# Kernel optimization log

Hardware: AMD Instinct MI355X
Metric: run time of the kernel (lower is better)

## Reference

```python
import math
import jax, jax.numpy as jnp
import numpy as np

T = 4096          # sequence length
H = 2048          # hidden_size
I = 8192          # intermediate_size = 4*H
LAYER_ID = 1
N_LAYERS = 24
EPS = 1e-5        # layer_norm_epsilon


def setup_inputs() -> dict:
    key = jax.random.key(0)
    ks = jax.random.split(key, 8)
    s = 1.0 / math.sqrt(H)
    si = 1.0 / math.sqrt(I)
    r0 = LAYER_ID / (N_LAYERS - 1)          # ratio_0_to_1
    r1 = 1.0 - LAYER_ID / N_LAYERS          # ratio_1_to_almost_0
    h = jnp.arange(H, dtype=jnp.float32)
    x = h / H
    time_decay = -5.0 + 8.0 * (h / (H - 1)) ** (0.7 + 1.3 * r0)
    zigzag = 0.5 * ((jnp.arange(1, H + 1) % 3).astype(jnp.float32) - 1.0)
    time_first = jnp.full((H,), math.log(0.3), jnp.float32) + zigzag
    tm_key = x ** r1
    tm_value = tm_key + 0.3 * r0
    tm_recep = x ** (0.5 * r1)
    return {
        "hidden": jax.random.normal(ks[0], (T, H), jnp.float32),
        "att_sx": jnp.zeros((H,), jnp.float32),
        "att_aa": jnp.zeros((H,), jnp.float32),
        "att_bb": jnp.zeros((H,), jnp.float32),
        "att_pp": jnp.full((H,), -1e30, jnp.float32),  # log-space -inf init
        "ffd_sx": jnp.zeros((H,), jnp.float32),
        "ln1_scale": jnp.ones((H,), jnp.float32),
        "ln1_bias": jnp.zeros((H,), jnp.float32),
        "ln2_scale": jnp.ones((H,), jnp.float32),
        "ln2_bias": jnp.zeros((H,), jnp.float32),
        "time_decay": time_decay.astype(jnp.float32),
        "time_first": time_first,
        "tm_key": tm_key.astype(jnp.float32),
        "tm_value": tm_value.astype(jnp.float32),
        "tm_recep": tm_recep.astype(jnp.float32),
        "Wk": jax.random.normal(ks[1], (H, H), jnp.float32) * s,
        "Wv": jax.random.normal(ks[2], (H, H), jnp.float32) * s,
        "Wr": jax.random.normal(ks[3], (H, H), jnp.float32) * s,
        "Wo": jax.random.normal(ks[4], (H, H), jnp.float32) * s,
        "ffn_tm_key": (x ** r1).astype(jnp.float32),
        "ffn_tm_recep": (x ** (0.5 * r1)).astype(jnp.float32),
        "Wfk": jax.random.normal(ks[5], (H, I), jnp.float32) * s,
        "Wfr": jax.random.normal(ks[6], (H, H), jnp.float32) * s,
        "Wfv": jax.random.normal(ks[7], (I, H), jnp.float32) * si,
    }


def _ln(x, scale, bias):
    mu = jnp.mean(x, axis=-1, keepdims=True)
    var = jnp.mean(jnp.square(x - mu), axis=-1, keepdims=True)
    return (x - mu) * jax.lax.rsqrt(var + EPS) * scale + bias


def _block(hidden, att_sx, att_aa, att_bb, att_pp, ffd_sx,
           ln1_scale, ln1_bias, ln2_scale, ln2_bias,
           time_decay, time_first, tm_key, tm_value, tm_recep,
           Wk, Wv, Wr, Wo, ffn_tm_key, ffn_tm_recep, Wfk, Wfr, Wfv):
    # ---- attention (WKV) sub-block ----
    x1 = _ln(hidden, ln1_scale, ln1_bias)               # [T,H]
    c_x = jnp.concatenate((att_sx[None, :], x1[:-1, :]), axis=0)  # token shift
    kx = x1 * tm_key + c_x * (1.0 - tm_key)
    vx = x1 * tm_value + c_x * (1.0 - tm_value)
    rx = x1 * tm_recep + c_x * (1.0 - tm_recep)
    r = jax.nn.sigmoid(rx @ Wr)                         # [T,H]
    k = kx @ Wk
    v = vx @ Wv
    w_decay = -jnp.exp(time_decay)                      # [H]

    def step(carry, kv):
        aa, bb, pp = carry
        kk, vv = kv
        ww = time_first + kk
        p = jnp.maximum(pp, ww)
        e1 = jnp.exp(pp - p)
        e2 = jnp.exp(ww - p)
        out_t = (e1 * aa + e2 * vv) / (e1 * bb + e2)
        ww2 = w_decay + pp
        p2 = jnp.maximum(ww2, kk)
        e1b = jnp.exp(ww2 - p2)
        e2b = jnp.exp(kk - p2)
        return (e1b * aa + e2b * vv, e1b * bb + e2b, p2), out_t

    (aa, bb, pp), cx = jax.lax.scan(step, (att_aa, att_bb, att_pp), (k, v))
    attention = x1 + (r * cx) @ Wo                      # inner residual (as in source)
    hidden2 = hidden + attention

    # ---- feed-forward (channel-mix) sub-block ----
    x2 = _ln(hidden2, ln2_scale, ln2_bias)
    sx2 = jnp.concatenate((ffd_sx[None, :], x2[:-1, :]), axis=0)
    fk = x2 * ffn_tm_key + sx2 * (1.0 - ffn_tm_key)
    fr = x2 * ffn_tm_recep + sx2 * (1.0 - ffn_tm_recep)
    rr = jax.nn.sigmoid(fr @ Wfr)
    kk2 = jnp.square(jax.nn.relu(fk @ Wfk))             # [T,I]
    ffn = rr * (kk2 @ Wfv)
    out = hidden2 + ffn
    return out, x1[-1, :], aa, bb, pp, x2[-1, :]


def reference(hidden, att_sx, att_aa, att_bb, att_pp, ffd_sx,
              ln1_scale, ln1_bias, ln2_scale, ln2_bias,
              time_decay, time_first, tm_key, tm_value, tm_recep,
              Wk, Wv, Wr, Wo, ffn_tm_key, ffn_tm_recep, Wfk, Wfr, Wfv):
    return _block(hidden, att_sx, att_aa, att_bb, att_pp, ffd_sx,
                  ln1_scale, ln1_bias, ln2_scale, ln2_bias,
                  time_decay, time_first, tm_key, tm_value, tm_recep,
                  Wk, Wv, Wr, Wo, ffn_tm_key, ffn_tm_recep, Wfk, Wfr, Wfv)
```

## Files before the change

### kernel.cpp

```cpp
#include <hip/hip_runtime.h>

#define T_SEQ 4096
#define HD 2048
#define ID 8192
#define LN_EPS 1e-5f
#define NCH 64
#define CHL 64
#define CHSZ ((size_t)NCH * HD)

typedef __attribute__((ext_vector_type(4))) float f32x4;
typedef __attribute__((ext_vector_type(8))) short short8;
typedef __attribute__((ext_vector_type(4))) unsigned short ushort4v;

#define GLB(p) ((const __attribute__((address_space(1))) void*)(p))
#define LDSP(p) ((__attribute__((address_space(3))) void*)(p))

__device__ __forceinline__ unsigned short f2bf(float f) {
  union { float f; unsigned int u; } x; x.f = f;
  unsigned int r = x.u + 0x7fffu + ((x.u >> 16) & 1u);
  return (unsigned short)(r >> 16);
}
__device__ __forceinline__ float bf2f(unsigned short u) {
  union { unsigned int i; float f; } x; x.i = ((unsigned int)u) << 16;
  return x.f;
}

__device__ __forceinline__ void wt_body(const float* __restrict__ W,
                                        unsigned short* __restrict__ Wt,
                                        int Nfull, int k_base, int n_base, int Kout) {
  __shared__ float tile[64][65];
  int tx = threadIdx.x, ty = threadIdx.y;
  int n0 = blockIdx.x * 64, k0 = blockIdx.y * 64;
#pragma unroll
  for (int j = 0; j < 8; ++j) {
    int k = ty + 8 * j;
    tile[k][tx] = W[(size_t)(k_base + k0 + k) * Nfull + n_base + n0 + tx];
  }
  __syncthreads();
#pragma unroll
  for (int j = 0; j < 8; ++j) {
    int n = ty + 8 * j;
    Wt[(size_t)(n0 + n) * Kout + k0 + tx] = f2bf(tile[tx][n]);
  }
}

__global__ void k_wt(const float* __restrict__ W, unsigned short* __restrict__ Wt) {
  wt_body(W, Wt, HD, 0, 0, HD);
}

__global__ void k_wt4(const float* __restrict__ W0, const float* __restrict__ W1,
                      const float* __restrict__ W2, const float* __restrict__ W3,
                      unsigned short* __restrict__ T) {
  const float* W = W0;
  if (blockIdx.z == 1) W = W1;
  else if (blockIdx.z == 2) W = W2;
  else if (blockIdx.z == 3) W = W3;
  wt_body(W, T + (size_t)blockIdx.z * HD * HD, HD, 0, 0, HD);
}

__global__ void k_wtB(const float* __restrict__ W, unsigned short* __restrict__ Wt,
                      int Nfull, int Kout, int kbz, int nbz, long dstz) {
  int z = blockIdx.z;
  wt_body(W, Wt + (size_t)z * dstz, Nfull, z * kbz, z * nbz, Kout);
}

__global__ void k_ln(const float* __restrict__ x, const float* __restrict__ sc,
                     const float* __restrict__ bi, unsigned short* __restrict__ y,
                     float* __restrict__ lastrow) {
  int row = blockIdx.x, tid = threadIdx.x;
  const float* xr = x + (size_t)row * HD;
  f32x4 v0 = *(const f32x4*)(xr + tid * 4);
  f32x4 v1 = *(const f32x4*)(xr + 1024 + tid * 4);
  float s = 0.f, s2 = 0.f;
#pragma unroll
  for (int q = 0; q < 4; ++q) { s += v0[q] + v1[q]; s2 += v0[q] * v0[q] + v1[q] * v1[q]; }
#pragma unroll
  for (int o = 32; o; o >>= 1) { s += __shfl_xor(s, o); s2 += __shfl_xor(s2, o); }
  __shared__ float red[8];
  int wv = tid >> 6;
  if ((tid & 63) == 0) { red[wv] = s; red[4 + wv] = s2; }
  __syncthreads();
  if (tid == 0) {
    float a = red[0] + red[1] + red[2] + red[3];
    float b = red[4] + red[5] + red[6] + red[7];
    float mu = a * (1.f / HD);
    float var = b * (1.f / HD) - mu * mu;
    red[0] = mu; red[1] = rsqrtf(var + LN_EPS);
  }
  __syncthreads();
  float mu = red[0], rs = red[1];
  f32x4 s0 = *(const f32x4*)(sc + tid * 4), s1 = *(const f32x4*)(sc + 1024 + tid * 4);
  f32x4 b0 = *(const f32x4*)(bi + tid * 4), b1 = *(const f32x4*)(bi + 1024 + tid * 4);
  float o0[4], o1[4];
  ushort4v y0, y1;
#pragma unroll
  for (int q = 0; q < 4; ++q) {
    o0[q] = (v0[q] - mu) * rs * s0[q] + b0[q];
    o1[q] = (v1[q] - mu) * rs * s1[q] + b1[q];
    y0[q] = f2bf(o0[q]); y1[q] = f2bf(o1[q]);
  }
  unsigned short* yr = y + (size_t)row * HD;
  *(ushort4v*)(yr + tid * 4) = y0;
  *(ushort4v*)(yr + 1024 + tid * 4) = y1;
  if (row == T_SEQ - 1) {
#pragma unroll
    for (int q = 0; q < 4; ++q) {
      lastrow[tid * 4 + q] = o0[q];
      lastrow[1024 + tid * 4 + q] = o1[q];
    }
  }
}

__global__ void k_mix_att(const unsigned short* __restrict__ x1, const float* __restrict__ sx,
                          const float* __restrict__ tk, const float* __restrict__ tv,
                          const float* __restrict__ tr,
                          unsigned short* __restrict__ kx, unsigned short* __restrict__ vx,
                          unsigned short* __restrict__ rx) {
  size_t idx = ((size_t)blockIdx.x * 256 + threadIdx.x) * 4;
  int h = (int)(idx & (HD - 1));
  ushort4v xu = *(const ushort4v*)(x1 + idx);
  f32x4 x, c;
#pragma unroll
  for (int q = 0; q < 4; ++q) x[q] = bf2f(xu[q]);
  if (idx >= HD) {
    ushort4v cu = *(const ushort4v*)(x1 + idx - HD);
#pragma unroll
    for (int q = 0; q < 4; ++q) c[q] = bf2f(cu[q]);
  } else {
    c = *(const f32x4*)(sx + h);
  }
  f32x4 a = *(const f32x4*)(tk + h);
  f32x4 b = *(const f32x4*)(tv + h);
  f32x4 r = *(const f32x4*)(tr + h);
  ushort4v ok, ov, orr;
#pragma unroll
  for (int q = 0; q < 4; ++q) {
    ok[q] = f2bf(x[q] * a[q] + c[q] * (1.f - a[q]));
    ov[q] = f2bf(x[q] * b[q] + c[q] * (1.f - b[q]));
    orr[q] = f2bf(x[q] * r[q] + c[q] * (1.f - r[q]));
  }
  *(ushort4v*)(kx + idx) = ok;
  *(ushort4v*)(vx + idx) = ov;
  *(ushort4v*)(rx + idx) = orr;
}

__global__ void k_mix_ffn(const unsigned short* __restrict__ x2, const float* __restrict__ sx,
                          const float* __restrict__ tk, const float* __restrict__ tr,
                          unsigned short* __restrict__ fk, unsigned short* __restrict__ fr) {
  size_t idx = ((size_t)blockIdx.x * 256 + threadIdx.x) * 4;
  int h = (int)(idx & (HD - 1));
  ushort4v xu = *(const ushort4v*)(x2 + idx);
  f32x4 x, c;
#pragma unroll
  for (int q = 0; q < 4; ++q) x[q] = bf2f(xu[q]);
  if (idx >= HD) {
    ushort4v cu = *(const ushort4v*)(x2 + idx - HD);
#pragma unroll
    for (int q = 0; q < 4; ++q) c[q] = bf2f(cu[q]);
  } else {
    c = *(const f32x4*)(sx + h);
  }
  f32x4 a = *(const f32x4*)(tk + h);
  f32x4 r = *(const f32x4*)(tr + h);
  ushort4v ok, orr;
#pragma unroll
  for (int q = 0; q < 4; ++q) {
    ok[q] = f2bf(x[q] * a[q] + c[q] * (1.f - a[q]));
    orr[q] = f2bf(x[q] * r[q] + c[q] * (1.f - r[q]));
  }
  *(ushort4v*)(fk + idx) = ok;
  *(ushort4v*)(fr + idx) = orr;
}

__global__ void k_scan1(const unsigned short* __restrict__ kb,
                        const unsigned short* __restrict__ vb,
                        const float* __restrict__ td, float* __restrict__ scr) {
  int c = blockIdx.x >> 3;
  int h = (blockIdx.x & 7) * 256 + threadIdx.x;
  float wd = -__expf(td[h]);
  float a = 0.f, b = 0.f, p = -1e30f;
  size_t base = (size_t)c * CHL * HD + h;
#pragma unroll 4
  for (int u = 0; u < CHL; ++u) {
    float kk = bf2f(kb[base]), vv = bf2f(vb[base]);
    base += HD;
    float ww2 = wd + p;
    float p2 = fmaxf(ww2, kk);
    float e1 = __expf(ww2 - p2), e2 = __expf(kk - p2);
    a = e1 * a + e2 * vv;
    b = e1 * b + e2;
    p = p2;
  }
  size_t i = (size_t)c * HD + h;
  scr[i] = a;
  scr[CHSZ + i] = b;
  scr[2 * CHSZ + i] = p;
}

__global__ void k_scan2(const float* __restrict__ scr, float* __restrict__ stscr,
                        const float* __restrict__ aa0, const float* __restrict__ bb0,
                        const float* __restrict__ pp0, const float* __restrict__ td,
                        float* __restrict__ st) {
  int h = blockIdx.x * 256 + threadIdx.x;
  float aa = aa0[h], bb = bb0[h], pp = pp0[h];
  float wdL = -__expf(td[h]) * (float)CHL;
  for (int c = 0; c < NCH; ++c) {
    size_t i = (size_t)c * HD + h;
    stscr[i] = aa;
    stscr[CHSZ + i] = bb;
    stscr[2 * CHSZ + i] = pp;
    float ca = scr[i], cb = scr[CHSZ + i], cp = scr[2 * CHSZ + i];
    float ww2 = wdL + pp;
    float p2 = fmaxf(ww2, cp);
    float e1 = __expf(ww2 - p2), e2 = __expf(cp - p2);
    aa = e1 * aa + e2 * ca;
    bb = e1 * bb + e2 * cb;
    pp = p2;
  }
  st[HD + h] = aa;
  st[2 * HD + h] = bb;
  st[3 * HD + h] = pp;
}

__global__ void k_scan3(const unsigned short* __restrict__ kb,
                        const unsigned short* __restrict__ vb,
                        const unsigned short* __restrict__ rb,
                        const float* __restrict__ tf_, const float* __restrict__ td,
                        const float* __restrict__ stscr, unsigned short* __restrict__ rcx) {
  int c = blockIdx.x >> 3;
  int h = (blockIdx.x & 7) * 256 + threadIdx.x;
  size_t i0 = (size_t)c * HD + h;
  float aa = stscr[i0], bb = stscr[CHSZ + i0], pp = stscr[2 * CHSZ + i0];
  float tf = tf_[h];
  float wd = -__expf(td[h]);
  size_t base = (size_t)c * CHL * HD + h;
#pragma unroll 4
  for (int u = 0; u < CHL; ++u) {
    float kk = bf2f(kb[base]), vv = bf2f(vb[base]), rv = bf2f(rb[base]);
    float ww = tf + kk;
    float p = fmaxf(pp, ww);
    float e1 = __expf(pp - p), e2 = __expf(ww - p);
    float cx = (e1 * aa + e2 * vv) / (e1 * bb + e2);
    rcx[base] = f2bf(rv * cx);
    float ww2 = wd + pp;
    float p2 = fmaxf(ww2, kk);
    float e1b = __expf(ww2 - p2), e2b = __expf(kk - p2);
    aa = e1b * aa + e2b * vv;
    bb = e1b * bb + e2b;
    pp = p2;
    base += HD;
  }
}

__global__ void k_fvred(float* __restrict__ out, const unsigned short* __restrict__ p0,
                        const unsigned short* __restrict__ p1) {
  size_t i = ((size_t)blockIdx.x * 256 + threadIdx.x) * 4;
  f32x4 o = *(f32x4*)(out + i);
  ushort4v a = *(const ushort4v*)(p0 + i);
  ushort4v b = *(const ushort4v*)(p1 + i);
#pragma unroll
  for (int q = 0; q < 4; ++q) o[q] += bf2f(a[q]) + bf2f(b[q]);
  *(f32x4*)(out + i) = o;
}

#define MFMA_Q(mh, nh, bset)                                                   \
  _Pragma("unroll") for (int i_ = 0; i_ < 4; ++i_)                             \
  _Pragma("unroll") for (int j_ = 0; j_ < 2; ++j_)                             \
  _Pragma("unroll") for (int ks_ = 0; ks_ < 2; ++ks_)                          \
    acc[(mh)*4 + i_][(nh)*2 + j_] = __builtin_amdgcn_mfma_f32_16x16x32_bf16(   \
        aS[i_ * 2 + ks_], bset[j_ * 2 + ks_], acc[(mh)*4 + i_][(nh)*2 + j_], 0, 0, 0);

#define RD_A(mh)                                                               \
  { const char* pa_ = Ab + arow0 + (mh)*8192;                                  \
    aS[0] = *(const short8*)(pa_ + 0 * 2048 + swz0);                           \
    aS[1] = *(const short8*)(pa_ + 0 * 2048 + swz1);                           \
    aS[2] = *(const short8*)(pa_ + 1 * 2048 + swz0);                           \
    aS[3] = *(const short8*)(pa_ + 1 * 2048 + swz1);                           \
    aS[4] = *(const short8*)(pa_ + 2 * 2048 + swz0);                           \
    aS[5] = *(const short8*)(pa_ + 2 * 2048 + swz1);                           \
    aS[6] = *(const short8*)(pa_ + 3 * 2048 + swz0);                           \
    aS[7] = *(const short8*)(pa_ + 3 * 2048 + swz1); }

#define RD_B(arr, nh)                                                          \
  { const char* pb_ = Bb + brow0 + (nh)*4096;                                  \
    arr[0] = *(const short8*)(pb_ + 0 * 2048 + swz0);                          \
    arr[1] = *(const short8*)(pb_ + 0 * 2048 + swz1);                          \
    arr[2] = *(const short8*)(pb_ + 1 * 2048 + swz0);                          \
    arr[3] = *(const short8*)(pb_ + 1 * 2048 + swz1); }

template <int EPI>
__global__ __launch_bounds__(512, 2) void k_gemm256(
    const unsigned short* __restrict__ A, const unsigned short* __restrict__ A1,
    const unsigned short* __restrict__ A2,
    const unsigned short* __restrict__ Bt, const unsigned short* __restrict__ Bt1,
    const unsigned short* __restrict__ Bt2,
    int M, int N, int K, int lda, int ldb,
    unsigned short* __restrict__ Cb, unsigned short* __restrict__ Cb1,
    unsigned short* __restrict__ Cb2, const unsigned short* __restrict__ E0b) {
  int koff = 0;
  if (EPI == 10) {
    koff = blockIdx.z * K;
    if (blockIdx.z) Cb = Cb1;
  } else {
    if (blockIdx.z == 1) { A = A1; Bt = Bt1; Cb = Cb1; }
    else if (blockIdx.z == 2) { A = A2; Bt = Bt2; Cb = Cb2; }
  }
  __shared__ char lds[131072];
  int tid = threadIdx.x;
  int wid = tid >> 6, lane = tid & 63;
  int row_l = lane & 15, kg = lane >> 4;
  int warp_m = wid >> 2, warp_n = wid & 3;
  int m0 = blockIdx.x * 256, n0 = blockIdx.y * 256;

  f32x4 acc[8][4];
#pragma unroll
  for (int i = 0; i < 8; ++i)
#pragma unroll
    for (int j = 0; j < 4; ++j)
#pragma unroll
      for (int q = 0; q < 4; ++q) acc[i][j][q] = 0.f;

  int srow = tid >> 3;
  int schunk = (tid & 7) ^ (srow & 7);
  const unsigned short* Asrc = A + (size_t)(m0 + srow) * lda + koff + schunk * 8;
  const unsigned short* Bsrc = Bt + (size_t)(n0 + srow) * ldb + koff + schunk * 8;
  char* ldsw = lds + wid * 1024;

  auto STAGE_A = [&](int d, int kt) {
#pragma unroll
    for (int h = 0; h < 2; ++h) {
      const unsigned short* s = Asrc + (size_t)(h * 128) * lda + kt;
      char* dst = ldsw + d * 65536 + h * 16384;
      __builtin_amdgcn_global_load_lds(GLB(s), LDSP(dst), 16, 0, 0);
      __builtin_amdgcn_global_load_lds(GLB(s + (size_t)64 * lda), LDSP(dst + 8192), 16, 0, 0);
    }
  };
  auto STAGE_B = [&](int d, int kt) {
#pragma unroll
    for (int h = 0; h < 2; ++h) {
      const unsigned short* s = Bsrc + (size_t)(h * 128) * ldb + kt;
      char* dst = ldsw + d * 65536 + 32768 + h * 16384;
      __builtin_amdgcn_global_load_lds(GLB(s), LDSP(dst), 16, 0, 0);
      __builtin_amdgcn_global_load_lds(GLB(s + (size_t)64 * ldb), LDSP(dst + 8192), 16, 0, 0);
    }
  };

  int swz0 = ((kg) ^ (row_l & 7)) << 4;
  int swz1 = ((4 + kg) ^ (row_l & 7)) << 4;
  int arow0 = (warp_m * 128 + row_l) * 128;
  int brow0 = (warp_n * 64 + row_l) * 128;

  short8 aS[8], b0[4], b1[4];
  int nt = K >> 6;
  STAGE_A(0, 0);
  STAGE_B(0, 0);

#pragma unroll 1
  for (int t = 0; t < nt; ++t) {
    int d = t & 1;
    const char* Ab = lds + d * 65536;
    const char* Bb = lds + d * 65536 + 32768;
    bool pre = (t + 1 < nt);
    int kn = (t + 1) << 6;
    if (pre) {
      STAGE_A(d ^ 1, kn);
      asm volatile("s_waitcnt vmcnt(4)" ::: "memory");
    } else {
      asm volatile("s_waitcnt vmcnt(0)" ::: "memory");
    }
    __builtin_amdgcn_s_barrier();
    RD_A(0)
    RD_B(b0, 0)
    asm volatile("s_waitcnt lgkmcnt(0)" ::: "memory");
    __builtin_amdgcn_s_setprio(1);
    MFMA_Q(0, 0, b0)
    __builtin_amdgcn_s_setprio(0);
    __builtin_amdgcn_s_barrier();
    if (pre) STAGE_B(d ^ 1, kn);
    RD_B(b1, 1)
    asm volatile("s_waitcnt lgkmcnt(0)" ::: "memory");
    __builtin_amdgcn_s_setprio(1);
    MFMA_Q(0, 1, b1)
    __builtin_amdgcn_s_setprio(0);
    __builtin_amdgcn_s_barrier();
    RD_A(1)
    asm volatile("s_waitcnt lgkmcnt(0)" ::: "memory");
    __builtin_amdgcn_s_setprio(1);
    MFMA_Q(1, 1, b1)
    __builtin_amdgcn_s_setprio(0);
    __builtin_amdgcn_s_barrier();
    __builtin_amdgcn_s_setprio(1);
    MFMA_Q(1, 0, b0)
    __builtin_amdgcn_s_setprio(0);
    __builtin_amdgcn_s_barrier();
  }

#pragma unroll
  for (int i = 0; i < 8; ++i) {
#pragma unroll
    for (int j = 0; j < 4; ++j) {
#pragma unroll
      for (int q = 0; q < 4; ++q) {
        int r = m0 + warp_m * 128 + i * 16 + kg * 4 + q;
        int c = n0 + warp_n * 64 + j * 16 + row_l;
        size_t idx = (size_t)r * N + c;
        float val = acc[i][j][q];
        if (EPI == 2) { float t2 = val > 0.f ? val * val : 0.f; Cb[idx] = f2bf(t2); }
        if (EPI == 8) {
          float o = (blockIdx.z == 2) ? 1.f / (1.f + __expf(-val)) : val;
          Cb[idx] = f2bf(o);
        }
        if (EPI == 10) Cb[idx] = f2bf(bf2f(E0b[idx]) * val);
      }
    }
  }
}

template <int EPI>
__global__ __launch_bounds__(512) void k_gemmB(
    const unsigned short* __restrict__ A, const unsigned short* __restrict__ Bt,
    int M, int N, int K, int lda, float* __restrict__ C,
    unsigned short* __restrict__ Cb, const float* __restrict__ E0,
    const unsigned short* __restrict__ E1b, const unsigned short* __restrict__ E0b) {
  __shared__ char lds[147456];
  int tid = threadIdx.x;
  int wid = tid >> 6, lane = tid & 63;
  int row_l = lane & 15, kg = lane >> 4;
  int warp_m = wid >> 2, warp_n = wid & 3;
  int m0 = blockIdx.x * 128, n0 = blockIdx.y * 256;

  f32x4 acc[4][4];
#pragma unroll
  for (int i = 0; i < 4; ++i)
#pragma unroll
    for (int j = 0; j < 4; ++j)
#pragma unroll
      for (int q = 0; q < 4; ++q) acc[i][j][q] = 0.f;

  int srow = tid >> 3;
  int schunk = (tid & 7) ^ (srow & 7);
  const unsigned short* Asrc = A + (size_t)(m0 + srow) * lda + schunk * 8;
  const unsigned short* Bsrc = Bt + (size_t)(n0 + srow) * K + schunk * 8;
  int wsw = wid * 1024;

  auto STAGE_P1 = [&](int d, int kt) {
    char* base = lds + d * 49152;
    __builtin_amdgcn_global_load_lds(GLB(Asrc + kt), LDSP(base + wsw), 16, 0, 0);
    __builtin_amdgcn_global_load_lds(GLB(Asrc + (size_t)64 * lda + kt),
                                     LDSP(base + 8192 + wsw), 16, 0, 0);
    __builtin_amdgcn_global_load_lds(GLB(Bsrc + kt), LDSP(base + 16384 + wsw), 16, 0, 0);
  };
  auto STAGE_P2 = [&](int d, int kt) {
    char* base = lds + d * 49152;
#pragma unroll
    for (int h = 1; h < 4; ++h)
      __builtin_amdgcn_global_load_lds(GLB(Bsrc + (size_t)(h * 64) * K + kt),
                                       LDSP(base + 16384 + h * 8192 + wsw), 16, 0, 0);
  };

  int swz0 = ((kg) ^ (row_l & 7)) << 4;
  int swz1 = ((4 + kg) ^ (row_l & 7)) << 4;
  int arow0 = (warp_m * 64 + row_l) * 128;
  int brow0 = (warp_n * 64 + row_l) * 128;

  short8 aS[8], b0[4], b1[4];
  int nt = K >> 6;
  STAGE_P1(0, 0); STAGE_P2(0, 0);
  STAGE_P1(1, 64); STAGE_P2(1, 64);

#pragma unroll 1
  for (int t = 0; t < nt; ++t) {
    int d = t % 3;
    const char* Ab = lds + d * 49152;
    const char* Bb = lds + d * 49152 + 16384;
    int b2 = t + 2 < nt ? (t + 2) % 3 : 0;
    int k2 = (t + 2) << 6;
    if (t + 2 < nt) {
      STAGE_P1(b2, k2);
      asm volatile("s_waitcnt vmcnt(9)" ::: "memory");
    } else if (t + 1 < nt) {
      asm volatile("s_waitcnt vmcnt(6)" ::: "memory");
    } else {
      asm volatile("s_waitcnt vmcnt(0)" ::: "memory");
    }
    __builtin_amdgcn_s_barrier();
    RD_A(0)
    RD_B(b0, 0)
    asm volatile("s_waitcnt lgkmcnt(0)" ::: "memory");
    __builtin_amdgcn_s_setprio(1);
    MFMA_Q(0, 0, b0)
    __builtin_amdgcn_s_setprio(0);
    __builtin_amdgcn_s_barrier();
    if (t + 2 < nt) STAGE_P2(b2, k2);
    RD_B(b1, 1)
    asm volatile("s_waitcnt lgkmcnt(0)" ::: "memory");
    __builtin_amdgcn_s_setprio(1);
    MFMA_Q(0, 1, b1)
    __builtin_amdgcn_s_setprio(0);
    __builtin_amdgcn_s_barrier();
  }

#pragma unroll
  for (int i = 0; i < 4; ++i) {
#pragma unroll
    for (int j = 0; j < 4; ++j) {
#pragma unroll
      for (int q = 0; q < 4; ++q) {
        int r = m0 + warp_m * 64 + i * 16 + kg * 4 + q;
        int c = n0 + warp_n * 64 + j * 16 + row_l;
        size_t idx = (size_t)r * N + c;
        float val = acc[i][j][q];
        if (EPI == 3) C[idx] = val + E0[idx] + bf2f(E1b[idx]);
        if (EPI == 6) Cb[idx] = f2bf(1.f / (1.f + __expf(-val)));
        if (EPI == 7) C[idx] += bf2f(E0b[idx]) * val;
      }
    }
  }
}

extern "C" void kernel_launch(void* const* d_in, const int* in_sizes, int n_in,
                              void* d_out, int out_size, void* d_ws, size_t ws_size,
                              hipStream_t stream) {
  (void)in_sizes; (void)n_in; (void)out_size;
  const float* hidden     = (const float*)d_in[0];
  const float* att_sx     = (const float*)d_in[1];
  const float* att_aa     = (const float*)d_in[2];
  const float* att_bb     = (const float*)d_in[3];
  const float* att_pp     = (const float*)d_in[4];
  const float* ffd_sx     = (const float*)d_in[5];
  const float* ln1_s      = (const float*)d_in[6];
  const float* ln1_b      = (const float*)d_in[7];
  const float* ln2_s      = (const float*)d_in[8];
  const float* ln2_b      = (const float*)d_in[9];
  const float* time_decay = (const float*)d_in[10];
  const float* time_first = (const float*)d_in[11];
  const float* tm_key     = (const float*)d_in[12];
  const float* tm_value   = (const float*)d_in[13];
  const float* tm_recep   = (const float*)d_in[14];
  const float* Wk         = (const float*)d_in[15];
  const float* Wv         = (const float*)d_in[16];
  const float* Wr         = (const float*)d_in[17];
  const float* Wo         = (const float*)d_in[18];
  const float* ffn_tm_key = (const float*)d_in[19];
  const float* ffn_tm_rec = (const float*)d_in[20];
  const float* Wfk        = (const float*)d_in[21];
  const float* Wfr        = (const float*)d_in[22];
  const float* Wfv        = (const float*)d_in[23];
  float* out = (float*)d_out;
  float* st = out + (size_t)T_SEQ * HD;

  const size_t MB8 = (size_t)HD * HD * 2;
  const size_t PG = (size_t)T_SEQ * HD * 2;
  char* w = (char*)d_ws;
  unsigned short* s0 = (unsigned short*)(w);
  unsigned short* s1 = (unsigned short*)(w + MB8);
  unsigned short* s2 = (unsigned short*)(w + 2 * MB8);
  unsigned short* s3 = (unsigned short*)(w + 3 * MB8);
  char* pA = w + 4 * MB8;
  char* pB = pA + PG;
  char* pC = pB + PG;
  char* pD = pC + PG;
  char* pE = pD + PG;
  char* pF = pE + PG;

  unsigned short* kx   = (unsigned short*)pA;
  unsigned short* vx   = (unsigned short*)pB;
  unsigned short* rx   = (unsigned short*)pC;
  unsigned short* kbf  = (unsigned short*)pD;
  unsigned short* x1bf = (unsigned short*)pE;
  unsigned short* vbf  = (unsigned short*)pF;
  unsigned short* rbf  = (unsigned short*)out;
  unsigned short* rcx  = (unsigned short*)pC;
  unsigned short* x2bf = (unsigned short*)pD;
  unsigned short* fk   = (unsigned short*)pF;
  unsigned short* fr   = (unsigned short*)pB;
  unsigned short* rr   = (unsigned short*)pA;
  unsigned short* kk2  = (unsigned short*)pB;
  unsigned short* pfv0 = (unsigned short*)pF;
  unsigned short* pfv1 = (unsigned short*)(w + 4 * MB8 + 6 * PG);
  float* scr   = (float*)s0;
  float* stscr = (float*)s1;
  bool big_ws = ws_size >= (size_t)(4 * MB8 + 7 * PG);

  dim3 tb64(64, 8);
  dim3 wg64(HD / 64, HD / 64);
  dim3 gB(T_SEQ / 128, HD / 256);

  k_wt4<<<dim3(HD / 64, HD / 64, 4), tb64, 0, stream>>>(Wk, Wv, Wr, Wo, s0);
  k_ln<<<T_SEQ, 256, 0, stream>>>(hidden, ln1_s, ln1_b, x1bf, st);
  k_mix_att<<<T_SEQ * HD / 1024, 256, 0, stream>>>(x1bf, att_sx, tm_key, tm_value, tm_recep,
                                                   kx, vx, rx);
  k_gemm256<8><<<dim3(T_SEQ / 256, HD / 256, 3), 512, 0, stream>>>(
      kx, vx, rx, s0, s1, s2, T_SEQ, HD, HD, HD, HD, kbf, vbf, rbf, nullptr);
  k_scan1<<<NCH * 8, 256, 0, stream>>>(kbf, vbf, time_decay, scr);
  k_scan2<<<HD / 256, 256, 0, stream>>>(scr, stscr, att_aa, att_bb, att_pp, time_decay, st);
  k_scan3<<<NCH * 8, 256, 0, stream>>>(kbf, vbf, rbf, time_first, time_decay, stscr, rcx);
  k_gemmB<3><<<gB, 512, 0, stream>>>(rcx, s3, T_SEQ, HD, HD, HD, out, nullptr,
                                     hidden, x1bf, nullptr);

  k_ln<<<T_SEQ, 256, 0, stream>>>(out, ln2_s, ln2_b, x2bf, st + 4 * HD);
  k_mix_ffn<<<T_SEQ * HD / 1024, 256, 0, stream>>>(x2bf, ffd_sx, ffn_tm_key, ffn_tm_rec,
                                                   fk, fr);
  k_wt<<<wg64, tb64, 0, stream>>>(Wfr, s3);
  k_gemmB<6><<<gB, 512, 0, stream>>>(fr, s3, T_SEQ, HD, HD, HD, nullptr, rr,
                                     nullptr, nullptr, nullptr);
  k_wtB<<<dim3(HD / 64, HD / 64, 4), tb64, 0, stream>>>(Wfk, s0, ID, HD, 0, 2048,
                                                        (long)2048 * 2048);
  k_gemm256<2><<<dim3(T_SEQ / 256, ID / 256), 512, 0, stream>>>(
      fk, nullptr, nullptr, s0, nullptr, nullptr, T_SEQ, ID, HD, HD, HD,
      kk2, nullptr, nullptr, nullptr);
  k_wtB<<<dim3(HD / 64, HD / 64, 4), tb64, 0, stream>>>(Wfv, s0, HD, ID, 2048, 0, 2048);
  if (big_ws) {
    k_gemm256<10><<<dim3(T_SEQ / 256, HD / 256, 2), 512, 0, stream>>>(
        kk2, nullptr, nullptr, s0, nullptr, nullptr, T_SEQ, HD, ID / 2, ID, ID,
        pfv0, pfv1, nullptr, rr);
    k_fvred<<<T_SEQ * HD / 1024, 256, 0, stream>>>(out, pfv0, pfv1);
  } else {
    k_gemmB<7><<<gB, 512, 0, stream>>>(kk2, s0, T_SEQ, HD, ID, ID, out, nullptr,
                                       nullptr, nullptr, rr);
  }
}
```

Baseline: 603.1 us.

## Add split-K GEMM variant with K=32 tiles, smaller LDS, higher occupancy

Replaces the templated EPI==10 split-K path of the FFN value GEMM with a dedicated kernel that stages 32-wide K tiles into a 64KB double-buffered LDS instead of 128KB. Launch bounds request 4 blocks per CU to raise occupancy and hide latency for the 128-block grid. Each iteration performs fewer MFMAs per barrier, so synchronisation overhead per FLOP rises, and register pressure at 4 waves/SIMD may cause spills.

```diff
diff --git a/kernel.cpp b/kernel.cpp
--- a/kernel.cpp
+++ b/kernel.cpp
@@ -296,15 +296,9 @@
     const unsigned short* __restrict__ Bt2,
     int M, int N, int K, int lda, int ldb,
     unsigned short* __restrict__ Cb, unsigned short* __restrict__ Cb1,
-    unsigned short* __restrict__ Cb2, const unsigned short* __restrict__ E0b) {
-  int koff = 0;
-  if (EPI == 10) {
-    koff = blockIdx.z * K;
-    if (blockIdx.z) Cb = Cb1;
-  } else {
-    if (blockIdx.z == 1) { A = A1; Bt = Bt1; Cb = Cb1; }
-    else if (blockIdx.z == 2) { A = A2; Bt = Bt2; Cb = Cb2; }
-  }
+    unsigned short* __restrict__ Cb2) {
+  if (blockIdx.z == 1) { A = A1; Bt = Bt1; Cb = Cb1; }
+  else if (blockIdx.z == 2) { A = A2; Bt = Bt2; Cb = Cb2; }
   __shared__ char lds[131072];
   int tid = threadIdx.x;
   int wid = tid >> 6, lane = tid & 63;
@@ -322,8 +316,8 @@
 
   int srow = tid >> 3;
   int schunk = (tid & 7) ^ (srow & 7);
-  const unsigned short* Asrc = A + (size_t)(m0 + srow) * lda + koff + schunk * 8;
-  const unsigned short* Bsrc = Bt + (size_t)(n0 + srow) * ldb + koff + schunk * 8;
+  const unsigned short* Asrc = A + (size_t)(m0 + srow) * lda + schunk * 8;
+  const unsigned short* Bsrc = Bt + (size_t)(n0 + srow) * ldb + schunk * 8;
   char* ldsw = lds + wid * 1024;
 
   auto STAGE_A = [&](int d, int kt) {
@@ -410,7 +404,108 @@
           float o = (blockIdx.z == 2) ? 1.f / (1.f + __expf(-val)) : val;
           Cb[idx] = f2bf(o);
         }
-        if (EPI == 10) Cb[idx] = f2bf(bf2f(E0b[idx]) * val);
+      }
+    }
+  }
+}
+
+__global__ __launch_bounds__(512, 4) void k_gemm256s(
+    const unsigned short* __restrict__ A, const unsigned short* __restrict__ Bt,
+    int M, int N, int K, int lda, int ldb,
+    unsigned short* __restrict__ Cb, unsigned short* __restrict__ Cb1,
+    const unsigned short* __restrict__ E0b) {
+  int koff = blockIdx.z * K;
+  if (blockIdx.z) Cb = Cb1;
+  __shared__ char lds[65536];
+  int tid = threadIdx.x;
+  int wid = tid >> 6, lane = tid & 63;
+  int row_l = lane & 15, kg = lane >> 4;
+  int warp_m = wid >> 2, warp_n = wid & 3;
+  int m0 = blockIdx.x * 256, n0 = blockIdx.y * 256;
+
+  f32x4 acc[8][4];
+#pragma unroll
+  for (int i = 0; i < 8; ++i)
+#pragma unroll
+    for (int j = 0; j < 4; ++j)
+#pragma unroll
+      for (int q = 0; q < 4; ++q) acc[i][j][q] = 0.f;
+
+  int srow = tid >> 2;
+  int schunk = (tid & 3) ^ (srow & 3);
+  const unsigned short* Asrc = A + (size_t)(m0 + srow) * lda + koff + schunk * 8;
+  const unsigned short* Bsrc = Bt + (size_t)(n0 + srow) * ldb + koff + schunk * 8;
+  char* ldsw = lds + wid * 1024;
+
+  auto STAGE = [&](int d, int kt) {
+    char* base = ldsw + d * 32768;
+    __builtin_amdgcn_global_load_lds(GLB(Asrc + kt), LDSP(base), 16, 0, 0);
+    __builtin_amdgcn_global_load_lds(GLB(Asrc + (size_t)128 * lda + kt),
+                                     LDSP(base + 8192), 16, 0, 0);
+    __builtin_amdgcn_global_load_lds(GLB(Bsrc + kt), LDSP(base + 16384), 16, 0, 0);
+    __builtin_amdgcn_global_load_lds(GLB(Bsrc + (size_t)128 * ldb + kt),
+                                     LDSP(base + 24576), 16, 0, 0);
+  };
+
+  int swz = ((kg) ^ (row_l & 3)) << 4;
+  int arow0 = warp_m * 8192 + row_l * 64;
+  int brow0 = 16384 + (warp_n >> 1) * 8192 + ((warp_n & 1) * 64 + row_l) * 64;
+
+  short8 aS[8], bF[4];
+  int nt = K >> 5;
+  STAGE(0, 0);
+
+#pragma unroll 1
+  for (int t = 0; t < nt; ++t) {
+    int d = t & 1;
+    const char* Ab = lds + d * 32768;
+    if (t + 1 < nt) {
+      STAGE(d ^ 1, (t + 1) << 5);
+      asm volatile("s_waitcnt vmcnt(4)" ::: "memory");
+    } else {
+      asm volatile("s_waitcnt vmcnt(0)" ::: "memory");
+    }
+    __builtin_amdgcn_s_barrier();
+#pragma unroll
+    for (int i = 0; i < 4; ++i)
+      aS[i] = *(const short8*)(Ab + arow0 + i * 1024 + swz);
+#pragma unroll
+    for (int j = 0; j < 4; ++j)
+      bF[j] = *(const short8*)(Ab + brow0 + j * 1024 + swz);
+    asm volatile("s_waitcnt lgkmcnt(0)" ::: "memory");
+    __builtin_amdgcn_s_setprio(1);
+#pragma unroll
+    for (int i = 0; i < 4; ++i)
+#pragma unroll
+      for (int j = 0; j < 4; ++j)
+        acc[i][j] = __builtin_amdgcn_mfma_f32_16x16x32_bf16(aS[i], bF[j], acc[i][j], 0, 0, 0);
+    __builtin_amdgcn_s_setprio(0);
+    __builtin_amdgcn_s_barrier();
+#pragma unroll
+    for (int i = 0; i < 4; ++i)
+      aS[4 + i] = *(const short8*)(Ab + arow0 + (4 + i) * 1024 + swz);
+    asm volatile("s_waitcnt lgkmcnt(0)" ::: "memory");
+    __builtin_amdgcn_s_setprio(1);
+#pragma unroll
+    for (int i = 0; i < 4; ++i)
+#pragma unroll
+      for (int j = 0; j < 4; ++j)
+        acc[4 + i][j] = __builtin_amdgcn_mfma_f32_16x16x32_bf16(aS[4 + i], bF[j],
+                                                               acc[4 + i][j], 0, 0, 0);
+    __builtin_amdgcn_s_setprio(0);
+    __builtin_amdgcn_s_barrier();
+  }
+
+#pragma unroll
+  for (int i = 0; i < 8; ++i) {
+#pragma unroll
+    for (int j = 0; j < 4; ++j) {
+#pragma unroll
+      for (int q = 0; q < 4; ++q) {
+        int r = m0 + warp_m * 128 + i * 16 + kg * 4 + q;
+        int c = n0 + warp_n * 64 + j * 16 + row_l;
+        size_t idx = (size_t)r * N + c;
+        Cb[idx] = f2bf(bf2f(E0b[idx]) * acc[i][j][q]);
       }
     }
   }
@@ -591,7 +686,7 @@
   k_mix_att<<<T_SEQ * HD / 1024, 256, 0, stream>>>(x1bf, att_sx, tm_key, tm_value, tm_recep,
                                                    kx, vx, rx);
   k_gemm256<8><<<dim3(T_SEQ / 256, HD / 256, 3), 512, 0, stream>>>(
-      kx, vx, rx, s0, s1, s2, T_SEQ, HD, HD, HD, HD, kbf, vbf, rbf, nullptr);
+      kx, vx, rx, s0, s1, s2, T_SEQ, HD, HD, HD, HD, kbf, vbf, rbf);
   k_scan1<<<NCH * 8, 256, 0, stream>>>(kbf, vbf, time_decay, scr);
   k_scan2<<<HD / 256, 256, 0, stream>>>(scr, stscr, att_aa, att_bb, att_pp, time_decay, st);
   k_scan3<<<NCH * 8, 256, 0, stream>>>(kbf, vbf, rbf, time_first, time_decay, stscr, rcx);
@@ -608,12 +703,11 @@
                                                         (long)2048 * 2048);
   k_gemm256<2><<<dim3(T_SEQ / 256, ID / 256), 512, 0, stream>>>(
       fk, nullptr, nullptr, s0, nullptr, nullptr, T_SEQ, ID, HD, HD, HD,
-      kk2, nullptr, nullptr, nullptr);
+      kk2, nullptr, nullptr);
   k_wtB<<<dim3(HD / 64, HD / 64, 4), tb64, 0, stream>>>(Wfv, s0, HD, ID, 2048, 0, 2048);
   if (big_ws) {
-    k_gemm256<10><<<dim3(T_SEQ / 256, HD / 256, 2), 512, 0, stream>>>(
-        kk2, nullptr, nullptr, s0, nullptr, nullptr, T_SEQ, HD, ID / 2, ID, ID,
-        pfv0, pfv1, nullptr, rr);
+    k_gemm256s<<<dim3(T_SEQ / 256, HD / 256, 2), 512, 0, stream>>>(
+        kk2, s0, T_SEQ, HD, ID / 2, ID, ID, pfv0, pfv1, rr);
     k_fvred<<<T_SEQ * HD / 1024, 256, 0, stream>>>(out, pfv0, pfv1);
   } else {
     k_gemmB<7><<<gB, 512, 0, stream>>>(kk2, s0, T_SEQ, HD, ID, ID, out, nullptr,
```

Result: slower. 1.495 ms (+147.8%).
